# Optimization experiments

Measured on AMD Instinct MI355X. Metric: run time of the kernel, lower is better.

## Reference

```python
import jax, jax.numpy as jnp
import numpy as np

B, H, W, D = 32, 56, 56, 192
WS, NH, SHIFT = 7, 6, 3
DH = D // NH          # head dim = 32
N = WS * WS           # 49 tokens per window
NW = (H // WS) * (W // WS)  # 64 windows per image
EPS = 1e-5


def _rel_pos_index():
    coords = np.stack(np.meshgrid(np.arange(WS), np.arange(WS), indexing='ij'))  # (2,WS,WS)
    flat = coords.reshape(2, -1)
    rel = flat[:, :, None] - flat[:, None, :]            # (2,N,N)
    rel = rel.transpose(1, 2, 0).astype(np.int64)        # (N,N,2)
    rel[..., 0] += WS - 1
    rel[..., 1] += WS - 1
    rel[..., 0] *= 2 * WS - 1
    return rel.sum(-1)                                    # (N,N) in [0,169)


def _shift_mask():
    img = np.zeros((H, W))
    bounds = [(0, H - WS), (H - WS, H - SHIFT), (H - SHIFT, H)]
    cnt = 0
    for h0, h1 in bounds:
        for w0, w1 in bounds:
            img[h0:h1, w0:w1] = cnt
            cnt += 1
    win = img.reshape(H // WS, WS, W // WS, WS).transpose(0, 2, 1, 3).reshape(-1, N)  # (nW,N)
    diff = win[:, None, :] - win[:, :, None]
    return np.where(diff != 0, -100.0, 0.0).astype(np.float32)  # (nW,N,N)


_REL_IDX = jnp.asarray(_rel_pos_index())
_MASK = jnp.asarray(_shift_mask())


def _layernorm(x, g, b):
    mu = jnp.mean(x, -1, keepdims=True)
    var = jnp.mean(jnp.square(x - mu), -1, keepdims=True)
    return (x - mu) * jax.lax.rsqrt(var + EPS) * g + b


def _window_partition(x):  # (B,H,W,C) -> (B*nW, N, C)
    Bx, _, _, C = x.shape
    x = x.reshape(Bx, H // WS, WS, W // WS, WS, C).transpose(0, 1, 3, 2, 4, 5)
    return x.reshape(-1, N, C)


def _window_reverse(w):  # (B*nW, N, C) -> (B,H,W,C)
    C = w.shape[-1]
    x = w.reshape(-1, H // WS, W // WS, WS, WS, C).transpose(0, 1, 3, 2, 4, 5)
    return x.reshape(-1, H, W, C)


def setup_inputs() -> dict:
    key = jax.random.key(0)
    ks = jax.random.split(key, 8)
    s = 0.02
    return {
        'x': jax.random.normal(ks[0], (B, H * W, D), jnp.float32),
        'norm1_g': jnp.ones((D,), jnp.float32),
        'norm1_b': jnp.zeros((D,), jnp.float32),
        'qkv_w': jax.random.normal(ks[1], (D, 3 * D), jnp.float32) * s,
        'qkv_b': jnp.zeros((3 * D,), jnp.float32),
        'proj_wo': jax.random.normal(ks[2], (D, D), jnp.float32) * s,
        'proj_bo': jnp.zeros((D,), jnp.float32),
        'rpb': jax.random.normal(ks[3], ((2 * WS - 1) ** 2, NH), jnp.float32) * s,
        'pl_w': jax.random.normal(ks[4], (NH, NH), jnp.float32) * s,
        'pl_b': jnp.zeros((NH,), jnp.float32),
        'pw_w': jax.random.normal(ks[5], (NH, NH), jnp.float32) * s,
        'pw_b': jnp.zeros((NH,), jnp.float32),
        'norm2_g': jnp.ones((D,), jnp.float32),
        'norm2_b': jnp.zeros((D,), jnp.float32),
        'fc1_w': jax.random.normal(ks[6], (D, 4 * D), jnp.float32) * s,
        'fc1_b': jnp.zeros((4 * D,), jnp.float32),
        'fc2_w': jax.random.normal(ks[7], (4 * D, D), jnp.float32) * s,
        'fc2_b': jnp.zeros((D,), jnp.float32),
    }


def reference(x, norm1_g, norm1_b, qkv_w, qkv_b, proj_wo, proj_bo, rpb,
              pl_w, pl_b, pw_w, pw_b, norm2_g, norm2_b,
              fc1_w, fc1_b, fc2_w, fc2_b):
    shortcut = x
    h = _layernorm(x, norm1_g, norm1_b).reshape(B, H, W, D)
    h = jnp.roll(h, (-SHIFT, -SHIFT), (1, 2))             # shifted windows
    win = _window_partition(h)                            # (B_, N, D), B_ = B*NW
    B_ = win.shape[0]

    qkv = win @ qkv_w + qkv_b                             # (B_, N, 3D)
    q_out, k_out, v_out = qkv[..., :D], qkv[..., D:2 * D], qkv[..., 2 * D:]
    qkv5 = qkv.reshape(B_, N, 3, NH, DH)
    q = qkv5[:, :, 0].transpose(0, 2, 1, 3)               # (B_, H, N, d)
    k = qkv5[:, :, 1].transpose(0, 2, 1, 3)
    v = qkv5[:, :, 2].transpose(0, 2, 1, 3)

    scale = DH ** -0.5
    attn = jnp.einsum('bhnd,bhmd->bhnm', q * scale, k)    # (B_, H, N, N)
    bias = rpb[_REL_IDX.reshape(-1)].reshape(N, N, NH).transpose(2, 0, 1)
    attn = attn + bias[None]
    # proj_l over the head axis (distillation transform, pre-softmax)
    attn = jnp.einsum('bhnm,hg->bgnm', attn, pl_w) + pl_b[None, :, None, None]
    # shifted-window mask
    attn = attn.reshape(B, NW, NH, N, N) + _MASK[None, :, None]
    attn = jax.nn.softmax(attn.reshape(B_, NH, N, N), axis=-1)
    # proj_w over the head axis (post-softmax)
    attn = jnp.einsum('bhnm,hg->bgnm', attn, pw_w) + pw_b[None, :, None, None]

    out = jnp.einsum('bhnm,bhmd->bnhd', attn, v).reshape(B_, N, D)
    out = out @ proj_wo + proj_bo

    h = _window_reverse(out)                              # (B,H,W,D)
    h = jnp.roll(h, (SHIFT, SHIFT), (1, 2)).reshape(B, H * W, D)
    xo = shortcut + h

    m = _layernorm(xo, norm2_g, norm2_b)
    m = jax.nn.gelu(m @ fc1_w + fc1_b, approximate=False) @ fc2_w + fc2_b
    xo = xo + m
    return xo, (q_out, k_out, v_out)
```

## Files before the change

kernel.cpp:

```cpp
#include <hip/hip_runtime.h>
#include <math.h>

#define TOK   100352
#define OUTCH 19267584L
#define NWIN  2048

typedef __attribute__((ext_vector_type(4))) float f32x4;
typedef __attribute__((ext_vector_type(8))) short bf16x8;

__device__ __forceinline__ unsigned short f2bf(float f) {
    unsigned u = __builtin_bit_cast(unsigned, f);
    u += 0x7FFFu + ((u >> 16) & 1u);
    return (unsigned short)(u >> 16);
}
__device__ __forceinline__ float bf2f(unsigned short s) {
    return __builtin_bit_cast(float, (unsigned)s << 16);
}

__global__ __launch_bounds__(256) void k_prep_w(const float* __restrict__ qkv_w,
                                                const float* __restrict__ proj_w,
                                                const float* __restrict__ fc1_w,
                                                const float* __restrict__ fc2_w,
                                                unsigned short* __restrict__ wt)
{
    int i = blockIdx.x * 256 + threadIdx.x;
    float v;
    if (i < 110592) {
        int instr = i >> 9, rem = i & 511, lane = rem >> 3, j = rem & 7;
        int ks = instr % 6, t = instr / 6;
        int ni = t & 1, t2 = t >> 1;
        int hh = t2 % 6, s = t2 / 6;
        int n = s * 192 + hh * 32 + ni * 16 + (lane & 15);
        int k = ks * 32 + ((lane >> 4) << 3) + j;
        v = qkv_w[k * 576 + n];
    } else if (i < 147456) {
        int j2 = i - 110592;
        int instr = j2 >> 9, rem = j2 & 511, lane = rem >> 3, j = rem & 7;
        int ks = instr % 6, t = instr / 6;
        int ni = t & 1, hh = t >> 1;
        int n = hh * 32 + ni * 16 + (lane & 15);
        int k = ks * 32 + ((lane >> 4) << 3) + j;
        v = proj_w[k * 192 + n];
    } else if (i < 294912) {
        int j2 = i - 147456;
        int instr = j2 >> 9, rem = j2 & 511, lane = rem >> 3, j = rem & 7;
        int ks = instr % 6, t = instr / 6;
        int ni = t % 3, t2 = t / 3;
        int wv = t2 & 3, s = t2 >> 2;
        int n = s * 192 + wv * 48 + ni * 16 + (lane & 15);
        int k = ks * 32 + ((lane >> 4) << 3) + j;
        v = fc1_w[k * 768 + n];
    } else {
        int j2 = i - 294912;
        int instr = j2 >> 9, rem = j2 & 511, lane = rem >> 3, j = rem & 7;
        int ks = instr % 6, t = instr / 6;
        int ni = t % 3, t2 = t / 3;
        int wv = t2 & 3, s = t2 >> 2;
        int n = wv * 48 + ni * 16 + (lane & 15);
        int k = s * 192 + ks * 32 + ((lane >> 4) << 3) + j;
        v = fc2_w[k * 192 + n];
    }
    wt[i] = f2bf(v);
}

__global__ __launch_bounds__(256) void k_mlp(const unsigned short* __restrict__ h2,
                                             const unsigned short* __restrict__ w1p,
                                             const float* __restrict__ b1,
                                             const unsigned short* __restrict__ w2p,
                                             const float* __restrict__ b2,
                                             const unsigned short* __restrict__ xv,
                                             float* __restrict__ xo)
{
    __shared__ unsigned short lA[64 * 192];
    __shared__ unsigned short lH[64 * 192];
    const int tid = threadIdx.x, lane = tid & 63, wv = tid >> 6;
    const long m0 = (long)blockIdx.x * 64;

    #pragma unroll
    for (int c = tid; c < 64 * 24; c += 256) {
        int row = c / 24, k16 = c - row * 24;
        bf16x8 v = *(const bf16x8*)(h2 + (m0 + row) * 192 + k16 * 8);
        *(bf16x8*)((char*)lA + row * 384 + ((k16 * 16) ^ ((row & 7) << 4))) = v;
    }

    f32x4 acc2[4][3];
    #pragma unroll
    for (int mi = 0; mi < 4; mi++)
        #pragma unroll
        for (int ni = 0; ni < 3; ni++) acc2[mi][ni] = (f32x4){0.f, 0.f, 0.f, 0.f};
    __syncthreads();

    for (int s = 0; s < 4; s++) {
        f32x4 acc1[4][3];
        #pragma unroll
        for (int mi = 0; mi < 4; mi++)
            #pragma unroll
            for (int ni = 0; ni < 3; ni++) acc1[mi][ni] = (f32x4){0.f, 0.f, 0.f, 0.f};
        #pragma unroll
        for (int ks = 0; ks < 6; ks++) {
            int kb = ks * 64 + ((lane >> 4) << 4);
            bf16x8 bfr[3];
            #pragma unroll
            for (int ni = 0; ni < 3; ni++) {
                int instr = ((s * 4 + wv) * 3 + ni) * 6 + ks;
                bfr[ni] = *(const bf16x8*)(w1p + (instr << 9) + (lane << 3));
            }
            #pragma unroll
            for (int mi = 0; mi < 4; mi++) {
                int row = mi * 16 + (lane & 15);
                bf16x8 afr = *(const bf16x8*)((char*)lA + row * 384 + (kb ^ ((row & 7) << 4)));
                #pragma unroll
                for (int ni = 0; ni < 3; ni++)
                    acc1[mi][ni] = __builtin_amdgcn_mfma_f32_16x16x32_bf16(afr, bfr[ni], acc1[mi][ni], 0, 0, 0);
            }
        }
        __syncthreads();
        #pragma unroll
        for (int mi = 0; mi < 4; mi++)
            #pragma unroll
            for (int ni = 0; ni < 3; ni++) {
                int col = wv * 48 + ni * 16 + (lane & 15);
                float bv = b1[s * 192 + col];
                #pragma unroll
                for (int r = 0; r < 4; r++) {
                    int row = mi * 16 + ((lane >> 4) << 2) + r;
                    float v = acc1[mi][ni][r] + bv;
                    float ge = 0.5f * v * (1.f + erff(v * 0.70710678118654752f));
                    *(unsigned short*)((char*)lH + row * 384 + ((2 * col) ^ ((row & 7) << 4))) = f2bf(ge);
                }
            }
        __syncthreads();
        #pragma unroll
        for (int ks = 0; ks < 6; ks++) {
            int kb = ks * 64 + ((lane >> 4) << 4);
            bf16x8 bfr[3];
            #pragma unroll
            for (int ni = 0; ni < 3; ni++) {
                int instr = ((s * 4 + wv) * 3 + ni) * 6 + ks;
                bfr[ni] = *(const bf16x8*)(w2p + (instr << 9) + (lane << 3));
            }
            #pragma unroll
            for (int mi = 0; mi < 4; mi++) {
                int row = mi * 16 + (lane & 15);
                bf16x8 afr = *(const bf16x8*)((char*)lH + row * 384 + (kb ^ ((row & 7) << 4)));
                #pragma unroll
                for (int ni = 0; ni < 3; ni++)
                    acc2[mi][ni] = __builtin_amdgcn_mfma_f32_16x16x32_bf16(afr, bfr[ni], acc2[mi][ni], 0, 0, 0);
            }
        }
    }
    #pragma unroll
    for (int mi = 0; mi < 4; mi++)
        #pragma unroll
        for (int ni = 0; ni < 3; ni++) {
            int gcol = wv * 48 + ni * 16 + (lane & 15);
            float bv = b2[gcol];
            #pragma unroll
            for (int r = 0; r < 4; r++) {
                long grow = m0 + mi * 16 + ((lane >> 4) << 2) + r;
                xo[grow * 192 + gcol] = bf2f(xv[grow * 192 + gcol]) + acc2[mi][ni][r] + bv;
            }
        }
}

#define ATS 67
#define QL_OFF 78800
#define KL_OFF 97616
#define VL_OFF 116432
__global__ __launch_bounds__(384) void k_attn(const float* __restrict__ x,
                                              const float* __restrict__ n1g,
                                              const float* __restrict__ n1b,
                                              const unsigned short* __restrict__ qkvp,
                                              const float* __restrict__ qbias,
                                              const float* __restrict__ rpb,
                                              const float* __restrict__ plw,
                                              const float* __restrict__ plb,
                                              const float* __restrict__ pww,
                                              const float* __restrict__ pwb,
                                              const unsigned short* __restrict__ projp,
                                              const float* __restrict__ pbias,
                                              const float* __restrict__ g2,
                                              const float* __restrict__ b2,
                                              float* __restrict__ outq,
                                              unsigned short* __restrict__ xv,
                                              unsigned short* __restrict__ h2)
{
    __shared__ __align__(16) char SM[136240];
    float (*ATT)[49][ATS] = (float(*)[49][ATS])SM;
    float (*xoT)[196]     = (float(*)[196])(SM + 19200);

    int w = blockIdx.x, widx = w & 63;
    int tid = threadIdx.x, lane = tid & 63, h = tid >> 6;
    int wi = widx >> 3, wj = widx & 7, bb = w >> 6;
    const long rowbase = (long)w * 49;
    const bool bdry = (wi == 7) || (wj == 7);

    if (tid < 196) {
        int r = tid >> 2, c0 = (tid & 3) * 48;
        int rr = r / 7, ss = r - rr * 7;
        int hh = wi * 7 + rr + 3; if (hh >= 56) hh -= 56;
        int ww = wj * 7 + ss + 3; if (ww >= 56) ww -= 56;
        const f32x4* sp = (const f32x4*)(x + ((long)(bb * 56 + hh) * 56 + ww) * 192 + c0);
        f32x4 vv[12];
        float sum = 0.f, sq = 0.f;
        #pragma unroll
        for (int i = 0; i < 12; i++) {
            vv[i] = sp[i];
            #pragma unroll
            for (int j = 0; j < 4; j++) { sum += vv[i][j]; sq += vv[i][j] * vv[i][j]; }
        }
        sum += __shfl_xor(sum, 1); sq += __shfl_xor(sq, 1);
        sum += __shfl_xor(sum, 2); sq += __shfl_xor(sq, 2);
        float mu = sum * (1.f / 192.f);
        float rs = rsqrtf(sq * (1.f / 192.f) - mu * mu + 1e-5f);
        #pragma unroll
        for (int i = 0; i < 6; i++) {
            bf16x8 o8;
            #pragma unroll
            for (int j = 0; j < 8; j++) {
                int idx = i * 8 + j, c = c0 + idx;
                o8[j] = (short)f2bf((vv[idx >> 2][idx & 3] - mu) * rs * n1g[c] + n1b[c]);
            }
            *(bf16x8*)(SM + r * 384 + ((2 * (c0 + i * 8)) ^ ((r & 7) << 4))) = o8;
        }
    }
    __syncthreads();

    f32x4 aq[4][2], ak[4][2], av[4][2];
    #pragma unroll
    for (int mi = 0; mi < 4; mi++)
        #pragma unroll
        for (int ni = 0; ni < 2; ni++) {
            aq[mi][ni] = (f32x4){0.f, 0.f, 0.f, 0.f};
            ak[mi][ni] = (f32x4){0.f, 0.f, 0.f, 0.f};
            av[mi][ni] = (f32x4){0.f, 0.f, 0.f, 0.f};
        }
    #pragma unroll
    for (int ks = 0; ks < 6; ks++) {
        int kb = ks * 64 + ((lane >> 4) << 4);
        bf16x8 afr[4];
        #pragma unroll
        for (int mi = 0; mi < 4; mi++) {
            int row = mi * 16 + (lane & 15);
            afr[mi] = *(const bf16x8*)(SM + row * 384 + (kb ^ ((row & 7) << 4)));
        }
        bf16x8 bq[2], bk[2], bv[2];
        #pragma unroll
        for (int ni = 0; ni < 2; ni++) {
            bq[ni] = *(const bf16x8*)(qkvp + (((((0 * 6 + h) * 2 + ni) * 6 + ks)) << 9) + (lane << 3));
            bk[ni] = *(const bf16x8*)(qkvp + (((((1 * 6 + h) * 2 + ni) * 6 + ks)) << 9) + (lane << 3));
            bv[ni] = *(const bf16x8*)(qkvp + (((((2 * 6 + h) * 2 + ni) * 6 + ks)) << 9) + (lane << 3));
        }
        #pragma unroll
        for (int mi = 0; mi < 4; mi++)
            #pragma unroll
            for (int ni = 0; ni < 2; ni++) {
                aq[mi][ni] = __builtin_amdgcn_mfma_f32_16x16x32_bf16(afr[mi], bq[ni], aq[mi][ni], 0, 0, 0);
                ak[mi][ni] = __builtin_amdgcn_mfma_f32_16x16x32_bf16(afr[mi], bk[ni], ak[mi][ni], 0, 0, 0);
                av[mi][ni] = __builtin_amdgcn_mfma_f32_16x16x32_bf16(afr[mi], bv[ni], av[mi][ni], 0, 0, 0);
            }
    }
    #pragma unroll
    for (int mi = 0; mi < 4; mi++)
        #pragma unroll
        for (int ni = 0; ni < 2; ni++) {
            int col = h * 32 + ni * 16 + (lane & 15);
            float bgq = qbias[col], bgk = qbias[192 + col], bgv = qbias[384 + col];
            #pragma unroll
            for (int r = 0; r < 4; r++) {
                int m = mi * 16 + ((lane >> 4) << 2) + r;
                if (m < 49) {
                    long gr = (rowbase + m) * 192 + col;
                    float fq = aq[mi][ni][r] + bgq;
                    float fk = ak[mi][ni][r] + bgk;
                    float fv = av[mi][ni][r] + bgv;
                    outq[gr] = fq; outq[OUTCH + gr] = fk; outq[2 * OUTCH + gr] = fv;
                    int sw = (2 * col) ^ ((m & 7) << 4);
                    *(unsigned short*)(SM + QL_OFF + m * 384 + sw) = f2bf(fq);
                    *(unsigned short*)(SM + KL_OFF + m * 384 + sw) = f2bf(fk);
                    *(unsigned short*)(SM + VL_OFF + m * 404 + 2 * col) = f2bf(fv);
                }
            }
        }
    __syncthreads();

    for (int c = tid; c < 6 * 49 * 15; c += 384) {
        int g = c / (49 * 15), rem = c - g * (49 * 15);
        int m = rem / 15, n = 49 + (rem - m * 15);
        ATT[g][m][n] = 0.f;
    }

    bf16x8 qfr[4], kfr[4];
    #pragma unroll
    for (int mi = 0; mi < 4; mi++) {
        int m = mi * 16 + (lane & 15); if (m > 48) m = 48;
        qfr[mi] = *(const bf16x8*)(SM + QL_OFF + m * 384 + ((h * 64 + ((lane >> 4) << 4)) ^ ((m & 7) << 4)));
    }
    #pragma unroll
    for (int ni = 0; ni < 4; ni++) {
        int n = ni * 16 + (lane & 15); if (n > 48) n = 48;
        kfr[ni] = *(const bf16x8*)(SM + KL_OFF + n * 384 + ((h * 64 + ((lane >> 4) << 4)) ^ ((n & 7) << 4)));
    }
    f32x4 sa[4][4];
    #pragma unroll
    for (int ni = 0; ni < 4; ni++)
        #pragma unroll
        for (int mi = 0; mi < 4; mi++)
            sa[mi][ni] = __builtin_amdgcn_mfma_f32_16x16x32_bf16(qfr[mi], kfr[ni], (f32x4){0.f, 0.f, 0.f, 0.f}, 0, 0, 0);
    const float scale = 0.17677669529663687f;
    #pragma unroll
    for (int mi = 0; mi < 4; mi++)
        #pragma unroll
        for (int ni = 0; ni < 4; ni++)
            #pragma unroll
            for (int r = 0; r < 4; r++) {
                int m = mi * 16 + ((lane >> 4) << 2) + r, n = ni * 16 + (lane & 15);
                if (m < 49 && n < 49) {
                    int rq = m / 7, cq = m - rq * 7, rk = n / 7, ck = n - rk * 7;
                    int ridx = (rq - rk + 6) * 13 + (cq - ck + 6);
                    ATT[h][m][n] = sa[mi][ni][r] * scale + rpb[ridx * 6 + h];
                }
            }
    __syncthreads();

    for (int p = tid; p < 2401; p += 384) {
        int m = p / 49, n = p - m * 49;
        float a[6];
        #pragma unroll
        for (int g = 0; g < 6; g++) a[g] = ATT[g][m][n];
        float msk = 0.f;
        if (bdry) {
            int rq = m / 7, cq = m - rq * 7, rk = n / 7, ck = n - rk * 7;
            int ghq = wi * 7 + rq, gwq = wj * 7 + cq, ghk = wi * 7 + rk, gwk = wj * 7 + ck;
            int regq = (ghq < 49 ? 0 : (ghq < 53 ? 1 : 2)) * 3 + (gwq < 49 ? 0 : (gwq < 53 ? 1 : 2));
            int regk = (ghk < 49 ? 0 : (ghk < 53 ? 1 : 2)) * 3 + (gwk < 49 ? 0 : (gwk < 53 ? 1 : 2));
            msk = (regq != regk) ? -100.f : 0.f;
        }
        #pragma unroll
        for (int g = 0; g < 6; g++) {
            float v = plb[g] + msk;
            #pragma unroll
            for (int h2i = 0; h2i < 6; h2i++) v += a[h2i] * plw[h2i * 6 + g];
            ATT[g][m][n] = v;
        }
    }
    __syncthreads();

    if (tid < 294) {
        int g = tid / 49, m = tid - g * 49;
        float* row = &ATT[g][m][0];
        float mx = row[0];
        #pragma unroll
        for (int j = 1; j < 49; j++) mx = fmaxf(mx, row[j]);
        float e[49]; float sm = 0.f;
        #pragma unroll
        for (int j = 0; j < 49; j++) { e[j] = __expf(row[j] - mx); sm += e[j]; }
        float inv = 1.f / sm;
        #pragma unroll
        for (int j = 0; j < 49; j++) row[j] = e[j] * inv;
    }
    __syncthreads();

    for (int p = tid; p < 2401; p += 384) {
        int m = p / 49, n = p - m * 49;
        float a[6];
        #pragma unroll
        for (int g = 0; g < 6; g++) a[g] = ATT[g][m][n];
        #pragma unroll
        for (int g = 0; g < 6; g++) {
            float v = pwb[g];
            #pragma unroll
            for (int h2i = 0; h2i < 6; h2i++) v += a[h2i] * pww[h2i * 6 + g];
            ATT[g][m][n] = v;
        }
    }
    __syncthreads();

    bf16x8 vfr[2][2];
    #pragma unroll
    for (int kst = 0; kst < 2; kst++)
        #pragma unroll
        for (int ni = 0; ni < 2; ni++) {
            int d = h * 32 + ni * 16 + (lane & 15);
            #pragma unroll
            for (int j = 0; j < 8; j++) {
                int n = kst * 32 + ((lane >> 4) << 3) + j; if (n > 48) n = 48;
                vfr[kst][ni][j] = *(const unsigned short*)(SM + VL_OFF + n * 404 + 2 * d);
            }
        }
    f32x4 oa[4][2];
    #pragma unroll
    for (int mi = 0; mi < 4; mi++)
        #pragma unroll
        for (int ni = 0; ni < 2; ni++) oa[mi][ni] = (f32x4){0.f, 0.f, 0.f, 0.f};
    #pragma unroll
    for (int kst = 0; kst < 2; kst++) {
        #pragma unroll
        for (int mi = 0; mi < 4; mi++) {
            int m = mi * 16 + (lane & 15); if (m > 48) m = 48;
            const float* ap = &ATT[h][m][kst * 32 + ((lane >> 4) << 3)];
            bf16x8 afr;
            #pragma unroll
            for (int j = 0; j < 8; j++) afr[j] = (short)f2bf(ap[j]);
            #pragma unroll
            for (int ni = 0; ni < 2; ni++)
                oa[mi][ni] = __builtin_amdgcn_mfma_f32_16x16x32_bf16(afr, vfr[kst][ni], oa[mi][ni], 0, 0, 0);
        }
    }
    __syncthreads();

    #pragma unroll
    for (int mi = 0; mi < 4; mi++)
        #pragma unroll
        for (int ni = 0; ni < 2; ni++)
            #pragma unroll
            for (int r = 0; r < 4; r++) {
                int m = mi * 16 + ((lane >> 4) << 2) + r;
                if (m < 49) {
                    int col = h * 32 + ni * 16 + (lane & 15);
                    *(unsigned short*)(SM + m * 384 + ((2 * col) ^ ((m & 7) << 4))) = f2bf(oa[mi][ni][r]);
                }
            }
    __syncthreads();

    f32x4 pacc[4][2];
    #pragma unroll
    for (int mi = 0; mi < 4; mi++)
        #pragma unroll
        for (int ni = 0; ni < 2; ni++) pacc[mi][ni] = (f32x4){0.f, 0.f, 0.f, 0.f};
    #pragma unroll
    for (int ks = 0; ks < 6; ks++) {
        int kb = ks * 64 + ((lane >> 4) << 4);
        bf16x8 bfr[2];
        #pragma unroll
        for (int ni = 0; ni < 2; ni++) {
            int instr = (h * 2 + ni) * 6 + ks;
            bfr[ni] = *(const bf16x8*)(projp + (instr << 9) + (lane << 3));
        }
        #pragma unroll
        for (int mi = 0; mi < 4; mi++) {
            int row = mi * 16 + (lane & 15); if (row > 48) row = 48;
            bf16x8 afr = *(const bf16x8*)(SM + row * 384 + (kb ^ ((row & 7) << 4)));
            #pragma unroll
            for (int ni = 0; ni < 2; ni++)
                pacc[mi][ni] = __builtin_amdgcn_mfma_f32_16x16x32_bf16(afr, bfr[ni], pacc[mi][ni], 0, 0, 0);
        }
    }

    #pragma unroll
    for (int mi = 0; mi < 4; mi++)
        #pragma unroll
        for (int ni = 0; ni < 2; ni++) {
            int gc = h * 32 + ni * 16 + (lane & 15);
            float bv = pbias[gc];
            #pragma unroll
            for (int r = 0; r < 4; r++) {
                int m = mi * 16 + ((lane >> 4) << 2) + r;
                if (m < 49) {
                    int rr = m / 7, ss = m - rr * 7;
                    int ho = wi * 7 + rr + 3; if (ho >= 56) ho -= 56;
                    int wo = wj * 7 + ss + 3; if (wo >= 56) wo -= 56;
                    long tp = ((long)(bb * 56 + ho) * 56 + wo);
                    xoT[m][gc] = x[tp * 192 + gc] + pacc[mi][ni][r] + bv;
                }
            }
        }
    __syncthreads();

    if (tid < 196) {
        int m = tid >> 2, c0 = (tid & 3) * 48;
        float vv[48];
        float sum = 0.f, sq = 0.f;
        #pragma unroll
        for (int i = 0; i < 48; i++) { vv[i] = xoT[m][c0 + i]; sum += vv[i]; sq += vv[i] * vv[i]; }
        sum += __shfl_xor(sum, 1); sq += __shfl_xor(sq, 1);
        sum += __shfl_xor(sum, 2); sq += __shfl_xor(sq, 2);
        float mu = sum * (1.f / 192.f);
        float rs = rsqrtf(sq * (1.f / 192.f) - mu * mu + 1e-5f);
        int rr = m / 7, ss = m - rr * 7;
        int ho = wi * 7 + rr + 3; if (ho >= 56) ho -= 56;
        int wo = wj * 7 + ss + 3; if (wo >= 56) wo -= 56;
        long tp = ((long)(bb * 56 + ho) * 56 + wo);
        #pragma unroll
        for (int i = 0; i < 6; i++) {
            bf16x8 o8, x8;
            #pragma unroll
            for (int j = 0; j < 8; j++) {
                int c = c0 + i * 8 + j;
                float xvf = vv[i * 8 + j];
                x8[j] = (short)f2bf(xvf);
                o8[j] = (short)f2bf((xvf - mu) * rs * g2[c] + b2[c]);
            }
            *(bf16x8*)(h2 + tp * 192 + c0 + i * 8) = o8;
            *(bf16x8*)(xv + tp * 192 + c0 + i * 8) = x8;
        }
    }
}

extern "C" void kernel_launch(void* const* d_in, const int* in_sizes, int n_in,
                              void* d_out, int out_size, void* d_ws, size_t ws_size,
                              hipStream_t stream)
{
    const float* x      = (const float*)d_in[0];
    const float* n1g    = (const float*)d_in[1];
    const float* n1b    = (const float*)d_in[2];
    const float* qkv_w  = (const float*)d_in[3];
    const float* qkv_b  = (const float*)d_in[4];
    const float* proj_w = (const float*)d_in[5];
    const float* proj_b = (const float*)d_in[6];
    const float* rpb    = (const float*)d_in[7];
    const float* pl_w   = (const float*)d_in[8];
    const float* pl_b   = (const float*)d_in[9];
    const float* pw_w   = (const float*)d_in[10];
    const float* pw_b   = (const float*)d_in[11];
    const float* n2g    = (const float*)d_in[12];
    const float* n2b    = (const float*)d_in[13];
    const float* fc1_w  = (const float*)d_in[14];
    const float* fc1_b  = (const float*)d_in[15];
    const float* fc2_w  = (const float*)d_in[16];
    const float* fc2_b  = (const float*)d_in[17];

    float* out   = (float*)d_out;
    float* out_q = out + OUTCH;

    char* ws = (char*)d_ws;
    unsigned short* bufT = (unsigned short*)ws;
    unsigned short* xvB  = (unsigned short*)(ws + 38535168);
    unsigned short* bufW = (unsigned short*)(ws + 2 * 38535168L);

    k_prep_w<<<1728, 256, 0, stream>>>(qkv_w, proj_w, fc1_w, fc2_w, bufW);
    k_attn<<<NWIN, 384, 0, stream>>>(x, n1g, n1b, bufW, qkv_b,
                                     rpb, pl_w, pl_b, pw_w, pw_b,
                                     bufW + 110592, proj_b, n2g, n2b,
                                     out_q, xvB, bufT);
    k_mlp<<<1568, 256, 0, stream>>>(bufT, bufW + 147456, fc1_b, bufW + 294912, fc2_b,
                                    xvB, out);
}
```

Baseline: 397.3 us.

## Store attention scores in bf16 and compact shared memory for higher occupancy

Changes the per-window attention score buffer from fp32 to bf16, overlays the Q/K/V staging regions onto the freed space, and shrinks shared memory from about 136KB to about 62KB. The launch bounds now request 3 blocks per CU so several windows can be resident at once and hide latency. The P·V fragment load becomes a single vector load instead of eight scalar loads plus conversions. Extra barriers are added to make the buffer aliasing safe. Rounding the pre-softmax and post-softmax scores and the head-mixing intermediates to bf16 reduces accuracy.

```diff
diff --git a/kernel.cpp b/kernel.cpp
--- a/kernel.cpp
+++ b/kernel.cpp
@@ -163,11 +163,11 @@
         }
 }
 
-#define ATS 67
-#define QL_OFF 78800
-#define KL_OFF 97616
-#define VL_OFF 116432
-__global__ __launch_bounds__(384) void k_attn(const float* __restrict__ x,
+#define ATS2 72
+#define KL_OFF 18816
+#define VL_OFF 42336
+#define XOT_OFF 18944
+__global__ __launch_bounds__(384, 3) void k_attn(const float* __restrict__ x,
                                               const float* __restrict__ n1g,
                                               const float* __restrict__ n1b,
                                               const unsigned short* __restrict__ qkvp,
@@ -185,9 +185,9 @@
                                               unsigned short* __restrict__ xv,
                                               unsigned short* __restrict__ h2)
 {
-    __shared__ __align__(16) char SM[136240];
-    float (*ATT)[49][ATS] = (float(*)[49][ATS])SM;
-    float (*xoT)[196]     = (float(*)[196])(SM + 19200);
+    __shared__ __align__(16) char SM[62144];
+    unsigned short (*ATT)[49][ATS2] = (unsigned short(*)[49][ATS2])SM;
+    float (*xoT)[196] = (float(*)[196])(SM + XOT_OFF);
 
     int w = blockIdx.x, widx = w & 63;
     int tid = threadIdx.x, lane = tid & 63, h = tid >> 6;
@@ -260,6 +260,8 @@
                 av[mi][ni] = __builtin_amdgcn_mfma_f32_16x16x32_bf16(afr[mi], bv[ni], av[mi][ni], 0, 0, 0);
             }
     }
+    __syncthreads();
+
     #pragma unroll
     for (int mi = 0; mi < 4; mi++)
         #pragma unroll
@@ -276,7 +278,7 @@
                     float fv = av[mi][ni][r] + bgv;
                     outq[gr] = fq; outq[OUTCH + gr] = fk; outq[2 * OUTCH + gr] = fv;
                     int sw = (2 * col) ^ ((m & 7) << 4);
-                    *(unsigned short*)(SM + QL_OFF + m * 384 + sw) = f2bf(fq);
+                    *(unsigned short*)(SM + m * 384 + sw) = f2bf(fq);
                     *(unsigned short*)(SM + KL_OFF + m * 384 + sw) = f2bf(fk);
                     *(unsigned short*)(SM + VL_OFF + m * 404 + 2 * col) = f2bf(fv);
                 }
@@ -284,29 +286,30 @@
         }
     __syncthreads();
 
+    bf16x8 qfr[4], kfr[4];
+    #pragma unroll
+    for (int mi = 0; mi < 4; mi++) {
+        int m = mi * 16 + (lane & 15); if (m > 48) m = 48;
+        qfr[mi] = *(const bf16x8*)(SM + m * 384 + ((h * 64 + ((lane >> 4) << 4)) ^ ((m & 7) << 4)));
+    }
+    #pragma unroll
+    for (int ni = 0; ni < 4; ni++) {
+        int n = ni * 16 + (lane & 15); if (n > 48) n = 48;
+        kfr[ni] = *(const bf16x8*)(SM + KL_OFF + n * 384 + ((h * 64 + ((lane >> 4) << 4)) ^ ((n & 7) << 4)));
+    }
+    f32x4 sa[4][4];
+    #pragma unroll
+    for (int ni = 0; ni < 4; ni++)
+        #pragma unroll
+        for (int mi = 0; mi < 4; mi++)
+            sa[mi][ni] = __builtin_amdgcn_mfma_f32_16x16x32_bf16(qfr[mi], kfr[ni], (f32x4){0.f, 0.f, 0.f, 0.f}, 0, 0, 0);
+    __syncthreads();
+
     for (int c = tid; c < 6 * 49 * 15; c += 384) {
         int g = c / (49 * 15), rem = c - g * (49 * 15);
         int m = rem / 15, n = 49 + (rem - m * 15);
-        ATT[g][m][n] = 0.f;
-    }
-
-    bf16x8 qfr[4], kfr[4];
-    #pragma unroll
-    for (int mi = 0; mi < 4; mi++) {
-        int m = mi * 16 + (lane & 15); if (m > 48) m = 48;
-        qfr[mi] = *(const bf16x8*)(SM + QL_OFF + m * 384 + ((h * 64 + ((lane >> 4) << 4)) ^ ((m & 7) << 4)));
-    }
-    #pragma unroll
-    for (int ni = 0; ni < 4; ni++) {
-        int n = ni * 16 + (lane & 15); if (n > 48) n = 48;
-        kfr[ni] = *(const bf16x8*)(SM + KL_OFF + n * 384 + ((h * 64 + ((lane >> 4) << 4)) ^ ((n & 7) << 4)));
-    }
-    f32x4 sa[4][4];
-    #pragma unroll
-    for (int ni = 0; ni < 4; ni++)
-        #pragma unroll
-        for (int mi = 0; mi < 4; mi++)
-            sa[mi][ni] = __builtin_amdgcn_mfma_f32_16x16x32_bf16(qfr[mi], kfr[ni], (f32x4){0.f, 0.f, 0.f, 0.f}, 0, 0, 0);
+        ATT[g][m][n] = 0;
+    }
     const float scale = 0.17677669529663687f;
     #pragma unroll
     for (int mi = 0; mi < 4; mi++)
@@ -318,7 +321,7 @@
                 if (m < 49 && n < 49) {
                     int rq = m / 7, cq = m - rq * 7, rk = n / 7, ck = n - rk * 7;
                     int ridx = (rq - rk + 6) * 13 + (cq - ck + 6);
-                    ATT[h][m][n] = sa[mi][ni][r] * scale + rpb[ridx * 6 + h];
+                    ATT[h][m][n] = f2bf(sa[mi][ni][r] * scale + rpb[ridx * 6 + h]);
                 }
             }
     __syncthreads();
@@ -327,7 +330,7 @@
         int m = p / 49, n = p - m * 49;
         float a[6];
         #pragma unroll
-        for (int g = 0; g < 6; g++) a[g] = ATT[g][m][n];
+        for (int g = 0; g < 6; g++) a[g] = bf2f(ATT[g][m][n]);
         float msk = 0.f;
         if (bdry) {
             int rq = m / 7, cq = m - rq * 7, rk = n / 7, ck = n - rk * 7;
@@ -341,23 +344,23 @@
             float v = plb[g] + msk;
             #pragma unroll
             for (int h2i = 0; h2i < 6; h2i++) v += a[h2i] * plw[h2i * 6 + g];
-            ATT[g][m][n] = v;
+            ATT[g][m][n] = f2bf(v);
         }
     }
     __syncthreads();
 
     if (tid < 294) {
         int g = tid / 49, m = tid - g * 49;
-        float* row = &ATT[g][m][0];
-        float mx = row[0];
-        #pragma unroll
-        for (int j = 1; j < 49; j++) mx = fmaxf(mx, row[j]);
+        unsigned short* row = &ATT[g][m][0];
+        float mx = bf2f(row[0]);
+        #pragma unroll
+        for (int j = 1; j < 49; j++) mx = fmaxf(mx, bf2f(row[j]));
         float e[49]; float sm = 0.f;
         #pragma unroll
-        for (int j = 0; j < 49; j++) { e[j] = __expf(row[j] - mx); sm += e[j]; }
+        for (int j = 0; j < 49; j++) { e[j] = __expf(bf2f(row[j]) - mx); sm += e[j]; }
         float inv = 1.f / sm;
         #pragma unroll
-        for (int j = 0; j < 49; j++) row[j] = e[j] * inv;
+        for (int j = 0; j < 49; j++) row[j] = f2bf(e[j] * inv);
     }
     __syncthreads();
 
@@ -365,13 +368,13 @@
         int m = p / 49, n = p - m * 49;
         float a[6];
         #pragma unroll
-        for (int g = 0; g < 6; g++) a[g] = ATT[g][m][n];
+        for (int g = 0; g < 6; g++) a[g] = bf2f(ATT[g][m][n]);
         #pragma unroll
         for (int g = 0; g < 6; g++) {
             float v = pwb[g];
             #pragma unroll
             for (int h2i = 0; h2i < 6; h2i++) v += a[h2i] * pww[h2i * 6 + g];
-            ATT[g][m][n] = v;
+            ATT[g][m][n] = f2bf(v);
         }
     }
     __syncthreads();
@@ -398,10 +401,7 @@
         #pragma unroll
         for (int mi = 0; mi < 4; mi++) {
             int m = mi * 16 + (lane & 15); if (m > 48) m = 48;
-            const float* ap = &ATT[h][m][kst * 32 + ((lane >> 4) << 3)];
-            bf16x8 afr;
-            #pragma unroll
-            for (int j = 0; j < 8; j++) afr[j] = (short)f2bf(ap[j]);
+            bf16x8 afr = *(const bf16x8*)&ATT[h][m][kst * 32 + ((lane >> 4) << 3)];
             #pragma unroll
             for (int ni = 0; ni < 2; ni++)
                 oa[mi][ni] = __builtin_amdgcn_mfma_f32_16x16x32_bf16(afr, vfr[kst][ni], oa[mi][ni], 0, 0, 0);
```

Measured after the change: 420.4 us. 5.8% more time.
